# Performance work log

Hardware: AMD Instinct MI355X
Metric: run time of the kernel (lower is better)

The kernel has to match this reference:

```python
import jax, jax.numpy as jnp
import numpy as np

N_SRC = 50000
N_DST = 50000
E = 640000
D_IN = 128
D_OUT = 128
H = 4
D_HEAD = D_OUT // H


def setup_inputs() -> dict:
    key = jax.random.key(0)
    k1, k2, k3, k4, k5, k6 = jax.random.split(key, 6)
    src_feat = jax.random.normal(k1, (N_SRC, D_IN), dtype=jnp.float32)
    dst_feat = jax.random.normal(k2, (N_DST, D_IN), dtype=jnp.float32)
    src_idx = jax.random.randint(k3, (E,), 0, N_SRC)
    dst_idx = jax.random.randint(k4, (E,), 0, N_DST)
    edge_index = jnp.stack([src_idx, dst_idx], axis=0)  # [2, E]
    # nn.Linear(d_in, d_out, bias=False): store as [d_in, d_out] so h = x @ W
    W = jax.random.normal(k5, (D_IN, D_OUT), dtype=jnp.float32) * (1.0 / np.sqrt(D_IN))
    # nn.Linear(2*d_head, 1, bias=False): attention vector of length 2*d_head
    a = jax.random.normal(k6, (2 * D_HEAD,), dtype=jnp.float32) * (1.0 / np.sqrt(2 * D_HEAD))
    return {"src_feat": src_feat, "dst_feat": dst_feat, "edge_index": edge_index,
            "W": W, "a": a, "num_dst": N_DST}


def reference(src_feat, dst_feat, edge_index, W, a, num_dst):
    # Dropout in eval mode (identity).
    d_out = W.shape[1]
    d_head = d_out // H
    src_idx = edge_index[0]
    dst_idx = edge_index[1]

    h_src = (src_feat @ W).reshape(-1, H, d_head)  # [N_src, H, d_head]
    h_dst = (dst_feat @ W).reshape(-1, H, d_head)  # [N_dst, H, d_head]
    h_src_e = h_src[src_idx]                        # [E, H, d_head]
    h_dst_e = h_dst[dst_idx]                        # [E, H, d_head]

    # a^T [h_src || h_dst] == h_src . a_src + h_dst . a_dst (shared across heads)
    a_src, a_dst = a[:d_head], a[d_head:]
    e = jax.nn.elu(jnp.einsum('ehd,d->eh', h_src_e, a_src)
                   + jnp.einsum('ehd,d->eh', h_dst_e, a_dst))  # [E, H]

    # Segment softmax over edges grouped by destination node.
    e_max = jax.ops.segment_max(e, dst_idx, num_segments=num_dst)      # [N_dst, H]
    exp_e = jnp.exp(e - e_max[dst_idx])
    denom = jax.ops.segment_sum(exp_e, dst_idx, num_segments=num_dst)  # [N_dst, H]
    alpha = exp_e / (denom[dst_idx] + 1e-12)                           # [E, H]

    # Scatter-add of weighted messages.
    out = jax.ops.segment_sum(alpha[..., None] * h_src_e, dst_idx,
                              num_segments=num_dst)                    # [N_dst, H, d_head]
    return out.reshape(num_dst, d_out)
```

## Files before the change

kernel.cpp:

```cpp
#include <hip/hip_runtime.h>
#include <math.h>

constexpr int N_SRC_ = 50000;
constexpr int N_DST_ = 50000;
constexpr int N_TOT_ = 100000;
constexpr int E_     = 640000;
constexpr int D_     = 128;
constexpr int DH_    = 32;
constexpr int CAP_   = 96;
constexpr int NTILES = N_TOT_ / 32;

static __device__ __forceinline__ unsigned short f2bf(float f) {
    unsigned int x = __float_as_uint(f);
    unsigned int r = (x + 0x7FFFu + ((x >> 16) & 1u)) >> 16;
    return (unsigned short)r;
}

__global__ __launch_bounds__(256) void k_transform(
    const float* __restrict__ src, const float* __restrict__ dst,
    const float* __restrict__ W, const float* __restrict__ a,
    unsigned short* __restrict__ h, float* __restrict__ s)
{
    __shared__ float wlds[128 * 128];
    __shared__ float alds[32 * 128];
    const int t = threadIdx.x;
    const int cg = t & 31;
    const int rg = t >> 5;
    const int head = cg >> 3;

    const float4* W4 = (const float4*)W;
    float4* wl4 = (float4*)wlds;
#pragma unroll
    for (int i = 0; i < 16; ++i) wl4[t + 256 * i] = W4[t + 256 * i];

    float4 ld[4];
    auto load_tile = [&](int tile) {
        int base = tile * 32;
#pragma unroll
        for (int i = 0; i < 4; ++i) {
            int q = t + 256 * i;
            int row = q >> 5, c4 = q & 31;
            int gr = base + row;
            float4 v = make_float4(0.f, 0.f, 0.f, 0.f);
            if (gr < N_TOT_) {
                const float* p = (gr < N_SRC_) ? (src + (size_t)gr * D_)
                                               : (dst + (size_t)(gr - N_SRC_) * D_);
                v = ((const float4*)p)[c4];
            }
            ld[i] = v;
        }
    };
    auto write_tile = [&]() {
        float4* al4 = (float4*)alds;
#pragma unroll
        for (int i = 0; i < 4; ++i) al4[t + 256 * i] = ld[i];
    };

    int tile = blockIdx.x;
    if (tile < NTILES) load_tile(tile);
    write_tile();
    __syncthreads();

    while (tile < NTILES) {
        int next = tile + gridDim.x;
        if (next < NTILES) load_tile(next);

        float acc[4][4] = {};
#pragma unroll 2
        for (int k = 0; k < 128; k += 4) {
            float4 av[4];
#pragma unroll
            for (int r = 0; r < 4; ++r)
                av[r] = *(const float4*)&alds[(rg + 8 * r) * 128 + k];
#pragma unroll
            for (int kk = 0; kk < 4; ++kk) {
                float4 wv = *(const float4*)&wlds[(k + kk) * 128 + 4 * cg];
#pragma unroll
                for (int r = 0; r < 4; ++r) {
                    float aa = (kk == 0) ? av[r].x : (kk == 1) ? av[r].y
                             : (kk == 2) ? av[r].z : av[r].w;
                    acc[r][0] = fmaf(aa, wv.x, acc[r][0]);
                    acc[r][1] = fmaf(aa, wv.y, acc[r][1]);
                    acc[r][2] = fmaf(aa, wv.z, acc[r][2]);
                    acc[r][3] = fmaf(aa, wv.w, acc[r][3]);
                }
            }
        }

        int base = tile * 32;
#pragma unroll
        for (int r = 0; r < 4; ++r) {
            int gr = base + rg + 8 * r;
            if (gr >= N_TOT_) continue;
            if (gr < N_SRC_) {
                ushort4 hv = make_ushort4(f2bf(acc[r][0]), f2bf(acc[r][1]),
                                          f2bf(acc[r][2]), f2bf(acc[r][3]));
                *(ushort4*)&h[(size_t)gr * D_ + 4 * cg] = hv;
            }
            const float* ah = (gr < N_SRC_) ? a : a + DH_;
            float4 av4 = *(const float4*)&ah[(cg & 7) * 4];
            float p = acc[r][0] * av4.x + acc[r][1] * av4.y
                    + acc[r][2] * av4.z + acc[r][3] * av4.w;
            p += __shfl_xor(p, 1, 64);
            p += __shfl_xor(p, 2, 64);
            p += __shfl_xor(p, 4, 64);
            if ((cg & 7) == 0) s[(size_t)gr * 4 + head] = p;
        }

        __syncthreads();
        if (next < NTILES) write_tile();
        __syncthreads();
        tile = next;
    }
}

__global__ __launch_bounds__(256) void k_scatter(
    const int* __restrict__ src_idx, const int* __restrict__ dst_idx,
    int* __restrict__ cursor, int* __restrict__ bucket)
{
    int e = blockIdx.x * 256 + threadIdx.x;
    if (e >= E_) return;
    int sn = src_idx[e], dn = dst_idx[e];
    int pos = atomicAdd(&cursor[dn], 1);
    if (pos < CAP_) bucket[(size_t)dn * CAP_ + pos] = sn;
}

__global__ __launch_bounds__(256) void k_gather(
    const unsigned int* __restrict__ h2,
    const float* __restrict__ s,
    const int* __restrict__ cursor, const int* __restrict__ bucket,
    float* __restrict__ out)
{
    int wid = (blockIdx.x * 256 + threadIdx.x) >> 6;
    int lane = threadIdx.x & 63;
    if (wid >= N_DST_) return;
    int cnt = min(cursor[wid], CAP_);
    const int hd = lane >> 4;
    const int sub = lane & 15;
    const float sd = s[(size_t)(N_SRC_ + wid) * 4 + hd];

    float2 acc = make_float2(0.f, 0.f);
    float den = 0.f;

    for (int base = 0; base < cnt; base += 64) {
        int rem = cnt - base; if (rem > 64) rem = 64;
        int bval = (lane < rem) ? bucket[(size_t)wid * CAP_ + base + lane] : 0;

        float wreg[4];
#pragma unroll
        for (int g = 0; g < 4; ++g) {
            int i = g * 16 + sub;
            int sn = __shfl(bval, i, 64);
            float x = s[(size_t)sn * 4 + hd] + sd;
            float eh = x > 0.f ? x : expm1f(x);
            float w = __expf(eh);
            wreg[g] = (i < rem) ? w : 0.f;
            den += wreg[g];
        }

#pragma unroll
        for (int g = 0; g < 4; ++g) {
            if (g * 16 >= rem) break;
#pragma unroll
            for (int ii = 0; ii < 16; ++ii) {
                int i = g * 16 + ii;
                if (i >= rem) break;
                int sn = __shfl(bval, i, 64);
                float w = __shfl(wreg[g], (hd << 4) + ii, 64);
                unsigned int v = h2[(size_t)sn * 64 + lane];
                float lo = __uint_as_float(v << 16);
                float hi = __uint_as_float(v & 0xFFFF0000u);
                acc.x = fmaf(w, lo, acc.x);
                acc.y = fmaf(w, hi, acc.y);
            }
        }
    }

    den += __shfl_xor(den, 1, 64);
    den += __shfl_xor(den, 2, 64);
    den += __shfl_xor(den, 4, 64);
    den += __shfl_xor(den, 8, 64);

    float inv = 1.f / (den + 1e-12f);
    *(float2*)&out[(size_t)wid * D_ + 2 * lane] =
        make_float2(acc.x * inv, acc.y * inv);
}

extern "C" void kernel_launch(void* const* d_in, const int* in_sizes, int n_in,
                              void* d_out, int out_size, void* d_ws, size_t ws_size,
                              hipStream_t stream)
{
    const float* src_feat = (const float*)d_in[0];
    const float* dst_feat = (const float*)d_in[1];
    const int*   edge     = (const int*)d_in[2];
    const int*   src_idx  = edge;
    const int*   dst_idx  = edge + E_;
    const float* W        = (const float*)d_in[3];
    const float* a        = (const float*)d_in[4];
    float*       out      = (float*)d_out;

    char* p = (char*)d_ws;
    auto alloc = [&](size_t bytes) {
        char* r = p;
        p += (bytes + 255) & ~(size_t)255;
        return r;
    };
    unsigned short* h = (unsigned short*)alloc((size_t)N_SRC_ * D_ * 2);
    float* s      = (float*)alloc((size_t)N_TOT_ * 4 * sizeof(float));
    int*   cursor = (int*)alloc((size_t)N_DST_ * sizeof(int));
    int*   bucket = (int*)alloc((size_t)N_DST_ * CAP_ * sizeof(int));

    hipMemsetAsync(cursor, 0, (size_t)N_DST_ * sizeof(int), stream);

    k_transform<<<512, 256, 0, stream>>>(src_feat, dst_feat, W, a, h, s);
    k_scatter<<<(E_ + 255) / 256, 256, 0, stream>>>(src_idx, dst_idx, cursor, bucket);
    k_gather<<<(N_DST_ * 64 + 255) / 256, 256, 0, stream>>>(
        (const unsigned int*)h, s, cursor, bucket, out);
}
```

Before: 252.8 us.

## Move feature transform to bf16x3 MFMA with folded attention-score columns

```diff
diff --git a/kernel.cpp b/kernel.cpp
--- a/kernel.cpp
+++ b/kernel.cpp
@@ -6,111 +6,145 @@
 constexpr int N_TOT_ = 100000;
 constexpr int E_     = 640000;
 constexpr int D_     = 128;
-constexpr int DH_    = 32;
 constexpr int CAP_   = 96;
-constexpr int NTILES = N_TOT_ / 32;
-
-static __device__ __forceinline__ unsigned short f2bf(float f) {
+constexpr int NCOL   = 144;
+constexpr int NTILE  = N_TOT_ / 32;
+
+typedef float f32x4  __attribute__((ext_vector_type(4)));
+typedef short bf16x8 __attribute__((ext_vector_type(8)));
+
+union U4 { unsigned int u[4]; bf16x8 v; };
+
+static __device__ __forceinline__ unsigned short f2bf_rne(float f) {
     unsigned int x = __float_as_uint(f);
-    unsigned int r = (x + 0x7FFFu + ((x >> 16) & 1u)) >> 16;
-    return (unsigned short)r;
-}
-
-__global__ __launch_bounds__(256) void k_transform(
+    return (unsigned short)((x + 0x7FFFu + ((x >> 16) & 1u)) >> 16);
+}
+
+__global__ __launch_bounds__(256) void k_prep(
+    const float* __restrict__ W, const float* __restrict__ a,
+    unsigned short* __restrict__ wt_hi, unsigned short* __restrict__ wt_lo)
+{
+    int tid = blockIdx.x * 256 + threadIdx.x;
+    if (tid >= NCOL * 16) return;
+    int n = tid >> 4, c = tid & 15;
+    int slot = c ^ (n & 15);
+    size_t base = (size_t)n * 128 + slot * 8;
+#pragma unroll
+    for (int j = 0; j < 8; ++j) {
+        int k = c * 8 + j;
+        float v = 0.f;
+        if (n < 128) {
+            v = W[(size_t)k * 128 + n];
+        } else if (n < 136) {
+            int half = (n - 128) >> 2, hd = (n - 128) & 3;
+            float acc = 0.f;
+            for (int c2 = 0; c2 < 32; ++c2)
+                acc += W[(size_t)k * 128 + hd * 32 + c2] * a[half * 32 + c2];
+            v = acc;
+        }
+        unsigned short hb = f2bf_rne(v);
+        float hf = __uint_as_float((unsigned int)hb << 16);
+        unsigned short lb = f2bf_rne(v - hf);
+        wt_hi[base + j] = hb;
+        wt_lo[base + j] = lb;
+    }
+}
+
+__global__ __launch_bounds__(256) void k_mm(
     const float* __restrict__ src, const float* __restrict__ dst,
-    const float* __restrict__ W, const float* __restrict__ a,
-    unsigned short* __restrict__ h, float* __restrict__ s)
-{
-    __shared__ float wlds[128 * 128];
-    __shared__ float alds[32 * 128];
+    const unsigned short* __restrict__ wt_hi, const unsigned short* __restrict__ wt_lo,
+    unsigned int* __restrict__ h, float* __restrict__ s)
+{
+    __shared__ unsigned short wl_hi[NCOL * 128];
+    __shared__ unsigned short wl_lo[NCOL * 128];
     const int t = threadIdx.x;
-    const int cg = t & 31;
-    const int rg = t >> 5;
-    const int head = cg >> 3;
-
-    const float4* W4 = (const float4*)W;
-    float4* wl4 = (float4*)wlds;
-#pragma unroll
-    for (int i = 0; i < 16; ++i) wl4[t + 256 * i] = W4[t + 256 * i];
-
-    float4 ld[4];
-    auto load_tile = [&](int tile) {
-        int base = tile * 32;
-#pragma unroll
-        for (int i = 0; i < 4; ++i) {
-            int q = t + 256 * i;
-            int row = q >> 5, c4 = q & 31;
-            int gr = base + row;
-            float4 v = make_float4(0.f, 0.f, 0.f, 0.f);
-            if (gr < N_TOT_) {
-                const float* p = (gr < N_SRC_) ? (src + (size_t)gr * D_)
-                                               : (dst + (size_t)(gr - N_SRC_) * D_);
-                v = ((const float4*)p)[c4];
-            }
-            ld[i] = v;
-        }
-    };
-    auto write_tile = [&]() {
-        float4* al4 = (float4*)alds;
-#pragma unroll
-        for (int i = 0; i < 4; ++i) al4[t + 256 * i] = ld[i];
-    };
-
-    int tile = blockIdx.x;
-    if (tile < NTILES) load_tile(tile);
-    write_tile();
+
+    {
+        const float4* gh = (const float4*)wt_hi;
+        const float4* gl = (const float4*)wt_lo;
+        float4* sh = (float4*)wl_hi;
+        float4* sl = (float4*)wl_lo;
+        for (int i = t; i < NCOL * 16; i += 256) { sh[i] = gh[i]; sl[i] = gl[i]; }
+    }
     __syncthreads();
 
-    while (tile < NTILES) {
-        int next = tile + gridDim.x;
-        if (next < NTILES) load_tile(next);
-
-        float acc[4][4] = {};
-#pragma unroll 2
-        for (int k = 0; k < 128; k += 4) {
-            float4 av[4];
-#pragma unroll
-            for (int r = 0; r < 4; ++r)
-                av[r] = *(const float4*)&alds[(rg + 8 * r) * 128 + k];
-#pragma unroll
-            for (int kk = 0; kk < 4; ++kk) {
-                float4 wv = *(const float4*)&wlds[(k + kk) * 128 + 4 * cg];
-#pragma unroll
-                for (int r = 0; r < 4; ++r) {
-                    float aa = (kk == 0) ? av[r].x : (kk == 1) ? av[r].y
-                             : (kk == 2) ? av[r].z : av[r].w;
-                    acc[r][0] = fmaf(aa, wv.x, acc[r][0]);
-                    acc[r][1] = fmaf(aa, wv.y, acc[r][1]);
-                    acc[r][2] = fmaf(aa, wv.z, acc[r][2]);
-                    acc[r][3] = fmaf(aa, wv.w, acc[r][3]);
+    const int wid = t >> 6, lane = t & 63;
+    const int g = lane >> 4, sidx = lane & 15;
+
+    for (int tile = blockIdx.x * 4 + wid; tile < NTILE; tile += gridDim.x * 4) {
+        const int base = tile * 32;
+        const int r0 = base + sidx, r1 = r0 + 16;
+        const float* p0 = (r0 < N_SRC_) ? src + (size_t)r0 * D_
+                                        : dst + (size_t)(r0 - N_SRC_) * D_;
+        const float* p1 = (r1 < N_SRC_) ? src + (size_t)r1 * D_
+                                        : dst + (size_t)(r1 - N_SRC_) * D_;
+
+        f32x4 acc[2][9];
+#pragma unroll
+        for (int m = 0; m < 2; ++m)
+#pragma unroll
+            for (int nf = 0; nf < 9; ++nf) acc[m][nf] = (f32x4)0.f;
+
+#pragma unroll
+        for (int ks = 0; ks < 4; ++ks) {
+            const int k0 = ks * 32 + g * 8;
+            bf16x8 ah[2], al[2];
+#pragma unroll
+            for (int m = 0; m < 2; ++m) {
+                const float* p = m ? p1 : p0;
+                float4 v0 = *(const float4*)(p + k0);
+                float4 v1 = *(const float4*)(p + k0 + 4);
+                float f[8] = {v0.x, v0.y, v0.z, v0.w, v1.x, v1.y, v1.z, v1.w};
+                U4 H, L;
+#pragma unroll
+                for (int q = 0; q < 4; ++q) {
+                    unsigned int x0 = __float_as_uint(f[2 * q]);
+                    unsigned int x1 = __float_as_uint(f[2 * q + 1]);
+                    unsigned int h0 = x0 & 0xFFFF0000u, h1 = x1 & 0xFFFF0000u;
+                    H.u[q] = (h0 >> 16) | h1;
+                    float rr0 = f[2 * q]     - __uint_as_float(h0);
+                    float rr1 = f[2 * q + 1] - __uint_as_float(h1);
+                    L.u[q] = (__float_as_uint(rr0) >> 16)
+                           | (__float_as_uint(rr1) & 0xFFFF0000u);
                 }
-            }
-        }
-
-        int base = tile * 32;
-#pragma unroll
-        for (int r = 0; r < 4; ++r) {
-            int gr = base + rg + 8 * r;
-            if (gr >= N_TOT_) continue;
-            if (gr < N_SRC_) {
-                ushort4 hv = make_ushort4(f2bf(acc[r][0]), f2bf(acc[r][1]),
-                                          f2bf(acc[r][2]), f2bf(acc[r][3]));
-                *(ushort4*)&h[(size_t)gr * D_ + 4 * cg] = hv;
-            }
-            const float* ah = (gr < N_SRC_) ? a : a + DH_;
-            float4 av4 = *(const float4*)&ah[(cg & 7) * 4];
-            float p = acc[r][0] * av4.x + acc[r][1] * av4.y
-                    + acc[r][2] * av4.z + acc[r][3] * av4.w;
-            p += __shfl_xor(p, 1, 64);
-            p += __shfl_xor(p, 2, 64);
-            p += __shfl_xor(p, 4, 64);
-            if ((cg & 7) == 0) s[(size_t)gr * 4 + head] = p;
-        }
-
-        __syncthreads();
-        if (next < NTILES) write_tile();
-        __syncthreads();
-        tile = next;
+                ah[m] = H.v; al[m] = L.v;
+            }
+#pragma unroll
+            for (int nf = 0; nf < 9; ++nf) {
+                const int n = nf * 16 + sidx;
+                const int off = n * 128 + ((ks * 4 + g) ^ sidx) * 8;
+                bf16x8 bh = *(const bf16x8*)&wl_hi[off];
+                bf16x8 bl = *(const bf16x8*)&wl_lo[off];
+                acc[0][nf] = __builtin_amdgcn_mfma_f32_16x16x32_bf16(ah[0], bh, acc[0][nf], 0, 0, 0);
+                acc[1][nf] = __builtin_amdgcn_mfma_f32_16x16x32_bf16(ah[1], bh, acc[1][nf], 0, 0, 0);
+                acc[0][nf] = __builtin_amdgcn_mfma_f32_16x16x32_bf16(al[0], bh, acc[0][nf], 0, 0, 0);
+                acc[1][nf] = __builtin_amdgcn_mfma_f32_16x16x32_bf16(al[1], bh, acc[1][nf], 0, 0, 0);
+                acc[0][nf] = __builtin_amdgcn_mfma_f32_16x16x32_bf16(ah[0], bl, acc[0][nf], 0, 0, 0);
+                acc[1][nf] = __builtin_amdgcn_mfma_f32_16x16x32_bf16(ah[1], bl, acc[1][nf], 0, 0, 0);
+            }
+        }
+
+#pragma unroll
+        for (int m = 0; m < 2; ++m) {
+            const int rowb = base + m * 16 + g * 4;
+#pragma unroll
+            for (int r = 0; r < 4; ++r) {
+                const int row = rowb + r;
+                if (sidx < 8) {
+                    int half = sidx >> 2, hd = sidx & 3;
+                    if ((row >= N_SRC_) == (half == 1))
+                        s[(size_t)row * 4 + hd] = acc[m][8][r];
+                }
+                if (row < N_SRC_) {
+#pragma unroll
+                    for (int q = 0; q < 4; ++q) {
+                        unsigned int val = (unsigned int)f2bf_rne(acc[m][2 * q][r])
+                                         | ((unsigned int)f2bf_rne(acc[m][2 * q + 1][r]) << 16);
+                        h[(size_t)row * 64 + q * 16 + sidx] = val;
+                    }
+                }
+            }
+        }
     }
 }
 
@@ -182,8 +216,8 @@
     den += __shfl_xor(den, 8, 64);
 
     float inv = 1.f / (den + 1e-12f);
-    *(float2*)&out[(size_t)wid * D_ + 2 * lane] =
-        make_float2(acc.x * inv, acc.y * inv);
+    out[(size_t)wid * D_ + 32 * hd + sub]      = acc.x * inv;
+    out[(size_t)wid * D_ + 32 * hd + sub + 16] = acc.y * inv;
 }
 
 extern "C" void kernel_launch(void* const* d_in, const int* in_sizes, int n_in,
@@ -205,15 +239,17 @@
         p += (bytes + 255) & ~(size_t)255;
         return r;
     };
-    unsigned short* h = (unsigned short*)alloc((size_t)N_SRC_ * D_ * 2);
+    unsigned int* h = (unsigned int*)alloc((size_t)N_SRC_ * 64 * 4);
     float* s      = (float*)alloc((size_t)N_TOT_ * 4 * sizeof(float));
     int*   cursor = (int*)alloc((size_t)N_DST_ * sizeof(int));
     int*   bucket = (int*)alloc((size_t)N_DST_ * CAP_ * sizeof(int));
+    unsigned short* wt_hi = (unsigned short*)alloc((size_t)NCOL * 128 * 2);
+    unsigned short* wt_lo = (unsigned short*)alloc((size_t)NCOL * 128 * 2);
 
     hipMemsetAsync(cursor, 0, (size_t)N_DST_ * sizeof(int), stream);
 
-    k_transform<<<512, 256, 0, stream>>>(src_feat, dst_feat, W, a, h, s);
+    k_prep<<<(NCOL * 16 + 255) / 256, 256, 0, stream>>>(W, a, wt_hi, wt_lo);
+    k_mm<<<512, 256, 0, stream>>>(src_feat, dst_feat, wt_hi, wt_lo, h, s);
     k_scatter<<<(E_ + 255) / 256, 256, 0, stream>>>(src_idx, dst_idx, cursor, bucket);
-    k_gather<<<(N_DST_ * 64 + 255) / 256, 256, 0, stream>>>(
-        (const unsigned int*)h, s, cursor, bucket, out);
-}
+    k_gather<<<(N_DST_ * 64 + 255) / 256, 256, 0, stream>>>(h, s, cursor, bucket, out);
+}
```

Measured after the change: 232.3 us. 1.09x faster.
